# Kernel optimization log

Measured on AMD Instinct MI355X. Metric: run time of the kernel, lower is better.

## Reference

```python
import jax, jax.numpy as jnp
import numpy as np

N, IN_DIM, OUT_DIM, HEADS = 4096, 256, 64, 8
NEG_SLOPE = 0.2
VERY_NEG = -1e9


def setup_inputs() -> dict:
    key = jax.random.key(0)
    k_x, k_adj, k_w, k_src, k_dst = jax.random.split(key, 5)
    x = jax.random.normal(k_x, (N, IN_DIM), dtype=jnp.float32)
    adjacency = jax.random.randint(k_adj, (N, N), 0, 2, dtype=jnp.int32)
    # xavier_uniform bounds
    def xavier(k, shape):
        fan_in, fan_out = shape[1], shape[0]
        lim = float(np.sqrt(6.0 / (fan_in + fan_out)))
        return jax.random.uniform(k, shape, jnp.float32, -lim, lim)
    W_proj = xavier(k_w, (OUT_DIM * HEADS, IN_DIM))  # torch Linear weight [out, in]
    attn_src = xavier(k_src, (HEADS, OUT_DIM))
    attn_dst = xavier(k_dst, (HEADS, OUT_DIM))
    bias = jnp.zeros((HEADS * OUT_DIM,), dtype=jnp.float32)
    return {"x": x, "adjacency": adjacency, "W_proj": W_proj,
            "attn_src": attn_src, "attn_dst": attn_dst, "bias": bias}


def reference(x, adjacency, W_proj, attn_src, attn_dst, bias):
    n = x.shape[0]
    h = (x @ W_proj.T).reshape(n, HEADS, OUT_DIM)          # [n, h, d]
    e_src = jnp.einsum('nhd,hd->nh', h, attn_src)           # [n, h]
    e_dst = jnp.einsum('nhd,hd->nh', h, attn_dst)           # [n, h]
    logits = e_src[:, None, :] + e_dst[None, :, :]          # [n, n, h]
    logits = jnp.where(logits >= 0, logits, NEG_SLOPE * logits)  # leaky_relu(0.2)
    mask = adjacency > 0                                    # [n, n]
    logits = jnp.where(mask[:, :, None], logits, VERY_NEG)
    alpha = jax.nn.softmax(logits, axis=1)                  # softmax over j (dim=1)
    out = jnp.einsum('ijh,jhd->ihd', alpha, h).reshape(n, HEADS * OUT_DIM)
    return out + bias
```

## Files before the change

### kernel.cpp

```cpp
#include <hip/hip_runtime.h>
#include <hip/hip_bf16.h>
#include <hip/hip_fp16.h>


#define GAT_N 4096
#define GAT_K 256
#define GAT_C 512
#define GAT_H 8
#define L2E 1.4426950408889634f
#define LN2 0.6931471805599453f

typedef _Float16 v8h __attribute__((ext_vector_type(8)));
typedef _Float16 f16x2 __attribute__((ext_vector_type(2)));
typedef float v4f __attribute__((ext_vector_type(4)));
typedef int v4i __attribute__((ext_vector_type(4)));

union U8 { v4i w; v8h h; };

static __device__ inline v4f mfma16(v8h a, v8h b, v4f c) {
    return __builtin_amdgcn_mfma_f32_16x16x32_f16(a, b, c, 0, 0, 0);
}

static __device__ inline unsigned pmax2(f16x2 e1, f16x2 e2, int f1w, int f2w) {
    f16x2 f1 = __builtin_bit_cast(f16x2, f1w);
    f16x2 f2 = __builtin_bit_cast(f16x2, f2w);
    f16x2 p1 = e1 * f1;
    f16x2 p2 = e2 * f2;
    f16x2 mx = __builtin_elementwise_max(p1, p2);
    return __builtin_bit_cast(unsigned, mx);
}

__global__ __launch_bounds__(256) void gat_prep(
    const float* __restrict__ x, const float* __restrict__ W,
    const float* __restrict__ asrc, const float* __restrict__ adst,
    const int* __restrict__ adj,
    _Float16* __restrict__ Hpack, float* __restrict__ ddata,
    float* __restrict__ esrc, unsigned* __restrict__ maskw)
{
    const int bid = blockIdx.x;
    const int tid = threadIdx.x;

    if (bid >= 512) {
        const int g = (bid - 512) * 4 + (tid >> 6);
        const int lane = tid & 63;
        const size_t base = (size_t)g * 2048;
        const int* pa = adj + base + (size_t)lane * 8;
        v4i v[8];
#pragma unroll
        for (int i = 0; i < 4; ++i) {
            v[2 * i]     = *(const v4i*)(pa + (size_t)i * 512);
            v[2 * i + 1] = *(const v4i*)(pa + (size_t)i * 512 + 4);
        }
#pragma unroll
        for (int i = 0; i < 4; ++i) {
            v4i a = v[2 * i], b = v[2 * i + 1];
            unsigned bits = (unsigned)(a.x > 0)        | ((unsigned)(a.y > 0) << 1)
                          | ((unsigned)(a.z > 0) << 2) | ((unsigned)(a.w > 0) << 3)
                          | ((unsigned)(b.x > 0) << 4) | ((unsigned)(b.y > 0) << 5)
                          | ((unsigned)(b.z > 0) << 6) | ((unsigned)(b.w > 0) << 7);
            unsigned w = bits << ((lane & 3) * 8);
            w |= __shfl_xor(w, 1);
            w |= __shfl_xor(w, 2);
            if ((lane & 3) == 0) maskw[(base >> 5) + i * 16 + (lane >> 2)] = w;
        }
        return;
    }

    const int head = bid & 7, mtile = bid >> 3;
    const int wv = tid >> 6, l = tid & 63;
    const int dlow = l & 15, q = l >> 4;
    const int rowbase = mtile * 64 + wv * 16;
    const int arow = rowbase + dlow;

    v4f acc[4] = {};
#pragma unroll
    for (int kc = 0; kc < 8; ++kc) {
        const int k0 = kc * 32 + q * 8;
        const float4* ap = (const float4*)(x + (size_t)arow * GAT_K + k0);
        float4 xa = ap[0], xb = ap[1];
        v8h af;
        af[0] = (_Float16)xa.x; af[1] = (_Float16)xa.y; af[2] = (_Float16)xa.z; af[3] = (_Float16)xa.w;
        af[4] = (_Float16)xb.x; af[5] = (_Float16)xb.y; af[6] = (_Float16)xb.z; af[7] = (_Float16)xb.w;
#pragma unroll
        for (int nt = 0; nt < 4; ++nt) {
            const int c = head * 64 + nt * 16 + dlow;
            const float4* bp = (const float4*)(W + (size_t)c * GAT_K + k0);
            float4 wa = bp[0], wb = bp[1];
            v8h bf;
            bf[0] = (_Float16)wa.x; bf[1] = (_Float16)wa.y; bf[2] = (_Float16)wa.z; bf[3] = (_Float16)wa.w;
            bf[4] = (_Float16)wb.x; bf[5] = (_Float16)wb.y; bf[6] = (_Float16)wb.z; bf[7] = (_Float16)wb.w;
            acc[nt] = mfma16(af, bf, acc[nt]);
        }
    }

    float as[4], ad[4];
#pragma unroll
    for (int nt = 0; nt < 4; ++nt) {
        const int d = nt * 16 + dlow;
        as[nt] = asrc[head * 64 + d];
        ad[nt] = adst[head * 64 + d];
    }
    float es[4], ed[4];
#pragma unroll
    for (int r = 0; r < 4; ++r) {
        float se = 0.f, de = 0.f;
#pragma unroll
        for (int nt = 0; nt < 4; ++nt) { se += acc[nt][r] * as[nt]; de += acc[nt][r] * ad[nt]; }
#pragma unroll
        for (int m = 1; m < 16; m <<= 1) { se += __shfl_xor(se, m); de += __shfl_xor(de, m); }
        es[r] = se; ed[r] = de;
    }
    if (dlow == 0) {
#pragma unroll
        for (int r = 0; r < 4; ++r) {
            const int j = rowbase + q * 4 + r;
            esrc[j * GAT_H + head] = es[r];
            ddata[(size_t)head * GAT_N + j] = ed[r] * L2E;
        }
    }

    const int jc = rowbase >> 5;
    const int p16 = rowbase & 16;
#pragma unroll
    for (int nt = 0; nt < 4; ++nt) {
#pragma unroll
        for (int rp = 0; rp < 4; rp += 2) {
            const int p = p16 + q * 4 + rp;
            const int qp = p >> 3, e = p & 7;
            const int lanep = qp * 16 + dlow;
            const size_t idx = ((((size_t)head * 128 + jc) * 4 + nt) * 64 + lanep) * 8 + e;
            union { unsigned u; _Float16 h[2]; } pk;
            pk.h[0] = (_Float16)acc[nt][rp];
            pk.h[1] = (_Float16)acc[nt][rp + 1];
            *(unsigned*)(Hpack + idx) = pk.u;
        }
    }
}

__global__ __launch_bounds__(256) void gat_ftab(
    const float* __restrict__ esrc, const float* __restrict__ ddata,
    unsigned* __restrict__ Epk1, unsigned* __restrict__ Epk2,
    _Float16* __restrict__ F1, _Float16* __restrict__ F2)
{
    __shared__ float wmax[4];
    const int bid = blockIdx.x;
    const int tid = threadIdx.x;
    const int head = bid >> 4;
    const float* dh = ddata + head * GAT_N;

    float m = -3.4e38f;
    {
        const v4f* dp = (const v4f*)(dh + tid * 16);
#pragma unroll
        for (int k = 0; k < 4; ++k) {
            v4f v = dp[k];
            m = fmaxf(m, fmaxf(fmaxf(v[0], v[1]), fmaxf(v[2], v[3])));
        }
    }
#pragma unroll
    for (int s = 1; s < 64; s <<= 1) m = fmaxf(m, __shfl_xor(m, s));
    if ((tid & 63) == 0) wmax[tid >> 6] = m;
    __syncthreads();
    const float Dml = fmaxf(fmaxf(wmax[0], wmax[1]), fmaxf(wmax[2], wmax[3]));
    const float Dm = Dml * LN2;

    const int i = (bid & 15) * 256 + tid;
    const int idx = head * GAT_N + i;
    const float s = esrc[i * GAT_H + head];
    const float sm = s + Dm;
    const float M = fmaxf(sm, 0.2f * sm);
    const float e1 = __builtin_amdgcn_exp2f((sm - M) * L2E);
    const float e2 = __builtin_amdgcn_exp2f((0.2f * sm - M) * L2E);
    union { _Float16 h[2]; unsigned u; } pk;
    pk.h[0] = (_Float16)e1; pk.h[1] = (_Float16)e1; Epk1[idx] = pk.u;
    pk.h[0] = (_Float16)e2; pk.h[1] = (_Float16)e2; Epk2[idx] = pk.u;
    const float dl = dh[i] - Dml;
    F1[idx] = (_Float16)__builtin_amdgcn_exp2f(dl);
    F2[idx] = (_Float16)__builtin_amdgcn_exp2f(0.2f * dl);
}

__global__ __launch_bounds__(256, 3) void gat_attn(
    const unsigned* __restrict__ maskw, const _Float16* __restrict__ Hpack,
    const unsigned* __restrict__ Epk1, const unsigned* __restrict__ Epk2,
    const _Float16* __restrict__ F1, const _Float16* __restrict__ F2,
    const float* __restrict__ bias, float* __restrict__ out)
{
    __shared__ __align__(16) char smem[2 * 64 * 81 * 4];
    unsigned (*mlds)[132] = (unsigned (*)[132])smem;
    float* xch = (float*)smem;

    const int bid = blockIdx.x;
    const int head = bid & 7;
    const int it = bid >> 3;
    const int tid = threadIdx.x;
    const int wv = tid >> 6, l = tid & 63;
    const int dlow = l & 15, q = l >> 4, qs = q * 8;
    const int ibase = it * 64;

    {
        const int r = tid >> 2;
        const int wq = (tid & 3) * 32;
        const unsigned* mp = maskw + (size_t)(ibase + r) * 128 + wq;
#pragma unroll
        for (int k = 0; k < 8; ++k) {
            v4i a = *(const v4i*)(mp + k * 4);
            *(v4i*)&mlds[r][wq + k * 4] = a;
        }
    }

    f16x2 E1p[4], E2p[4];
#pragma unroll
    for (int g = 0; g < 4; ++g) {
        E1p[g] = __builtin_bit_cast(f16x2, Epk1[head * GAT_N + ibase + g * 16 + dlow]);
        E2p[g] = __builtin_bit_cast(f16x2, Epk2[head * GAT_N + ibase + g * 16 + dlow]);
    }

    v4f accW[4][4] = {};
    v4f accZ[4] = {};
    v8h ones;
#pragma unroll
    for (int e = 0; e < 8; ++e) ones[e] = (_Float16)1.0f;

    const _Float16* Hl = Hpack + (size_t)head * 262144 + (size_t)l * 8;
    const _Float16* F1h = F1 + head * GAT_N;
    const _Float16* F2h = F2 + head * GAT_N;

    __syncthreads();

    v8h Ah[4], Bh[4];

#define GAT_LOADH(P, T) {                                                    \
        const _Float16* hp_ = Hl + (size_t)((T) * 4 + wv) * 2048;            \
        P##h[0] = *(const v8h*)(hp_);                                        \
        P##h[1] = *(const v8h*)(hp_ + 512);                                  \
        P##h[2] = *(const v8h*)(hp_ + 1024);                                 \
        P##h[3] = *(const v8h*)(hp_ + 1536);                                 \
    }

#define GAT_COMP(P, T) {                                                     \
        const int jc_ = (T) * 4 + wv;                                        \
        const int kg_ = (jc_ << 5) + qs;                                     \
        const v4i f1_ = *(const v4i*)(F1h + kg_);                            \
        const v4i f2_ = *(const v4i*)(F2h + kg_);                            \
        _Pragma("unroll")                                                    \
        for (int g = 0; g < 4; ++g) {                                        \
            const unsigned mw_ = mlds[g * 16 + dlow][jc_];                   \
            const unsigned b8_ = (mw_ >> qs) & 255u;                         \
            const unsigned z1_ = (((b8_ & 15u) * 0x204081u) << 7) & 0x80808080u; \
            const unsigned z2_ = (((b8_ >> 4) * 0x204081u) << 7) & 0x80808080u;  \
            const unsigned m1_ = (z1_ >> 7) * 255u;                          \
            const unsigned m2_ = (z2_ >> 7) * 255u;                          \
            U8 fr_;                                                          \
            fr_.w[0] = (int)(pmax2(E1p[g], E2p[g], f1_[0], f2_[0])           \
                             & __builtin_amdgcn_perm(0u, m1_, 0x01010000u)); \
            fr_.w[1] = (int)(pmax2(E1p[g], E2p[g], f1_[1], f2_[1])           \
                             & __builtin_amdgcn_perm(0u, m1_, 0x03030202u)); \
            fr_.w[2] = (int)(pmax2(E1p[g], E2p[g], f1_[2], f2_[2])           \
                             & __builtin_amdgcn_perm(0u, m2_, 0x01010000u)); \
            fr_.w[3] = (int)(pmax2(E1p[g], E2p[g], f1_[3], f2_[3])           \
                             & __builtin_amdgcn_perm(0u, m2_, 0x03030202u)); \
            accW[g][0] = mfma16(fr_.h, P##h[0], accW[g][0]);                 \
            accW[g][1] = mfma16(fr_.h, P##h[1], accW[g][1]);                 \
            accW[g][2] = mfma16(fr_.h, P##h[2], accW[g][2]);                 \
            accW[g][3] = mfma16(fr_.h, P##h[3], accW[g][3]);                 \
            accZ[g]    = mfma16(fr_.h, ones,  accZ[g]);                      \
        }                                                                    \
    }

    GAT_LOADH(A, 0)
    for (int t = 0; t < 30; t += 2) {
        GAT_LOADH(B, t + 1)
        GAT_COMP(A, t)
        GAT_LOADH(A, t + 2)
        GAT_COMP(B, t + 1)
    }
    GAT_LOADH(B, 31)
    GAT_COMP(A, 30)
    GAT_COMP(B, 31)
#undef GAT_LOADH
#undef GAT_COMP

    __syncthreads();
    {
        float* xb = xch + ((size_t)(wv >> 1) * 64 + l) * 81;
        if (wv & 1) {
#pragma unroll
            for (int g = 0; g < 4; ++g) {
#pragma unroll
                for (int nt = 0; nt < 4; ++nt)
#pragma unroll
                    for (int r = 0; r < 4; ++r) xb[(g * 4 + nt) * 4 + r] = accW[g][nt][r];
#pragma unroll
                for (int r = 0; r < 4; ++r) xb[64 + g * 4 + r] = accZ[g][r];
            }
        }
        __syncthreads();
        if (!(wv & 1)) {
#pragma unroll
            for (int g = 0; g < 4; ++g) {
#pragma unroll
                for (int nt = 0; nt < 4; ++nt)
#pragma unroll
                    for (int r = 0; r < 4; ++r) accW[g][nt][r] += xb[(g * 4 + nt) * 4 + r];
#pragma unroll
                for (int r = 0; r < 4; ++r) accZ[g][r] += xb[64 + g * 4 + r];
            }
        }
        __syncthreads();
        float* x0 = xch + (size_t)l * 81;
        if (wv == 2) {
#pragma unroll
            for (int g = 0; g < 4; ++g) {
#pragma unroll
                for (int nt = 0; nt < 4; ++nt)
#pragma unroll
                    for (int r = 0; r < 4; ++r) x0[(g * 4 + nt) * 4 + r] = accW[g][nt][r];
#pragma unroll
                for (int r = 0; r < 4; ++r) x0[64 + g * 4 + r] = accZ[g][r];
            }
        }
        __syncthreads();
        if (wv == 0) {
#pragma unroll
            for (int g = 0; g < 4; ++g) {
#pragma unroll
                for (int nt = 0; nt < 4; ++nt)
#pragma unroll
                    for (int r = 0; r < 4; ++r) accW[g][nt][r] += x0[(g * 4 + nt) * 4 + r];
#pragma unroll
                for (int r = 0; r < 4; ++r) accZ[g][r] += x0[64 + g * 4 + r];
            }
#pragma unroll
            for (int g = 0; g < 4; ++g) {
                float zi[4];
#pragma unroll
                for (int r = 0; r < 4; ++r) zi[r] = 1.0f / accZ[g][r];
#pragma unroll
                for (int nt = 0; nt < 4; ++nt) {
                    const int col = head * 64 + nt * 16 + dlow;
                    const float b = bias[col];
#pragma unroll
                    for (int r = 0; r < 4; ++r) {
                        const int row = ibase + g * 16 + q * 4 + r;
                        out[(size_t)row * GAT_C + col] = accW[g][nt][r] * zi[r] + b;
                    }
                }
            }
        }
    }
}

extern "C" void kernel_launch(void* const* d_in, const int* in_sizes, int n_in,
                              void* d_out, int out_size, void* d_ws, size_t ws_size,
                              hipStream_t stream) {
    const float* x    = (const float*)d_in[0];
    const int*   adj  = (const int*)d_in[1];
    const float* W    = (const float*)d_in[2];
    const float* asrc = (const float*)d_in[3];
    const float* adst = (const float*)d_in[4];
    const float* bias = (const float*)d_in[5];
    float* out = (float*)d_out;

    char* ws = (char*)d_ws;
    _Float16* Hpack  = (_Float16*)ws;
    unsigned* maskw  = (unsigned*)(ws + (4u << 20));
    float*    ddata  = (float*)(ws + (6u << 20));
    float*    esrc   = (float*)(ws + (6u << 20) + (128u << 10));
    unsigned* Epk1   = (unsigned*)(ws + (6u << 20) + (256u << 10));
    unsigned* Epk2   = (unsigned*)(ws + (6u << 20) + (384u << 10));
    _Float16* F1     = (_Float16*)(ws + (6u << 20) + (512u << 10));
    _Float16* F2     = (_Float16*)(ws + (6u << 20) + (576u << 10));

    hipLaunchKernelGGL(gat_prep, dim3(2560), dim3(256), 0, stream,
                       x, W, asrc, adst, adj, Hpack, ddata, esrc, maskw);
    hipLaunchKernelGGL(gat_ftab, dim3(128), dim3(256), 0, stream,
                       esrc, ddata, Epk1, Epk2, F1, F2);
    hipLaunchKernelGGL(gat_attn, dim3(512), dim3(256), 0, stream,
                       maskw, Hpack, Epk1, Epk2, F1, F2, bias, out);
}
```

Before: 64.89 us.

## Split projection K across waves with LDS reduction and interleave mask blocks

The projection part of gat_prep now assigns one 16-row tile per block and splits the K dimension across the four waves. Partial accumulators are reduced through shared memory, which raises the projection block count from 512 to 2048. Mask-packing blocks are interleaved with projection blocks (even/odd block IDs) so both kinds of work are spread across CUs. The cost is more x/W reloads per block, an LDS reduction plus a barrier, and three waves that sit idle after the reduction.

```diff
diff --git a/kernel.cpp b/kernel.cpp
--- a/kernel.cpp
+++ b/kernel.cpp
@@ -37,11 +37,12 @@
     _Float16* __restrict__ Hpack, float* __restrict__ ddata,
     float* __restrict__ esrc, unsigned* __restrict__ maskw)
 {
+    __shared__ float red[3][64][17];
     const int bid = blockIdx.x;
     const int tid = threadIdx.x;
 
-    if (bid >= 512) {
-        const int g = (bid - 512) * 4 + (tid >> 6);
+    if ((bid & 1) == 0) {
+        const int g = (bid >> 1) * 4 + (tid >> 6);
         const int lane = tid & 63;
         const size_t base = (size_t)g * 2048;
         const int* pa = adj + base + (size_t)lane * 8;
@@ -66,16 +67,17 @@
         return;
     }
 
-    const int head = bid & 7, mtile = bid >> 3;
+    const int pb = bid >> 1;
+    const int head = pb & 7, t16 = pb >> 3;
     const int wv = tid >> 6, l = tid & 63;
     const int dlow = l & 15, q = l >> 4;
-    const int rowbase = mtile * 64 + wv * 16;
+    const int rowbase = t16 * 16;
     const int arow = rowbase + dlow;
 
     v4f acc[4] = {};
 #pragma unroll
-    for (int kc = 0; kc < 8; ++kc) {
-        const int k0 = kc * 32 + q * 8;
+    for (int kc2 = 0; kc2 < 2; ++kc2) {
+        const int k0 = (wv * 2 + kc2) * 32 + q * 8;
         const float4* ap = (const float4*)(x + (size_t)arow * GAT_K + k0);
         float4 xa = ap[0], xb = ap[1];
         v8h af;
@@ -93,6 +95,24 @@
         }
     }
 
+    if (wv != 0) {
+        float* rp = &red[wv - 1][l][0];
+#pragma unroll
+        for (int nt = 0; nt < 4; ++nt)
+#pragma unroll
+            for (int r = 0; r < 4; ++r) rp[nt * 4 + r] = acc[nt][r];
+    }
+    __syncthreads();
+    if (wv != 0) return;
+#pragma unroll
+    for (int p = 0; p < 3; ++p) {
+        const float* rp = &red[p][l][0];
+#pragma unroll
+        for (int nt = 0; nt < 4; ++nt)
+#pragma unroll
+            for (int r = 0; r < 4; ++r) acc[nt][r] += rp[nt * 4 + r];
+    }
+
     float as[4], ad[4];
 #pragma unroll
     for (int nt = 0; nt < 4; ++nt) {
@@ -124,14 +144,14 @@
 #pragma unroll
     for (int nt = 0; nt < 4; ++nt) {
 #pragma unroll
-        for (int rp = 0; rp < 4; rp += 2) {
-            const int p = p16 + q * 4 + rp;
+        for (int rp2 = 0; rp2 < 4; rp2 += 2) {
+            const int p = p16 + q * 4 + rp2;
             const int qp = p >> 3, e = p & 7;
             const int lanep = qp * 16 + dlow;
             const size_t idx = ((((size_t)head * 128 + jc) * 4 + nt) * 64 + lanep) * 8 + e;
             union { unsigned u; _Float16 h[2]; } pk;
-            pk.h[0] = (_Float16)acc[nt][rp];
-            pk.h[1] = (_Float16)acc[nt][rp + 1];
+            pk.h[0] = (_Float16)acc[nt][rp2];
+            pk.h[1] = (_Float16)acc[nt][rp2 + 1];
             *(unsigned*)(Hpack + idx) = pk.u;
         }
     }
@@ -371,7 +391,7 @@
     _Float16* F1     = (_Float16*)(ws + (6u << 20) + (512u << 10));
     _Float16* F2     = (_Float16*)(ws + (6u << 20) + (576u << 10));
 
-    hipLaunchKernelGGL(gat_prep, dim3(2560), dim3(256), 0, stream,
+    hipLaunchKernelGGL(gat_prep, dim3(4096), dim3(256), 0, stream,
                        x, W, asrc, adst, adj, Hpack, ddata, esrc, maskw);
     hipLaunchKernelGGL(gat_ftab, dim3(128), dim3(256), 0, stream,
                        esrc, ddata, Epk1, Epk2, F1, F2);
```

New measurement: 75.87 us. +16.9%, slower.
